# Optimization experiments

Hardware: AMD Instinct MI355X
Metric: run time of the kernel (lower is better)

Reference implementation:

```python
import jax, jax.numpy as jnp
import numpy as np

N_LAYERS = 2
D_MODEL = 1024
D_INNER = 2048  # expand=2
D_STATE = 16
D_CONV = 4
DT_RANK = 64    # ceil(d_model/16)
N_CLASSES = 10
B, L = 4, 1024


def setup_inputs() -> dict:
    key = jax.random.key(0)
    ks = jax.random.split(key, 20)
    s = 0.02
    inp = {
        'x': jax.random.normal(ks[0], (B, L, D_MODEL), jnp.float32),
        'ln1_w': jnp.ones((N_LAYERS, D_MODEL), jnp.float32),
        'ln1_b': jnp.zeros((N_LAYERS, D_MODEL), jnp.float32),
        'in_proj_w': jax.random.normal(ks[1], (N_LAYERS, 2 * D_INNER, D_MODEL), jnp.float32) * s,
        'conv_w': jax.random.normal(ks[2], (N_LAYERS, D_INNER, D_CONV), jnp.float32) * 0.2,
        'conv_b': jnp.zeros((N_LAYERS, D_INNER), jnp.float32),
        'x_proj_w': jax.random.normal(ks[3], (N_LAYERS, DT_RANK + 2 * D_STATE, D_INNER), jnp.float32) * s,
        'dt_proj_w': jax.random.normal(ks[4], (N_LAYERS, D_INNER, DT_RANK), jnp.float32) * 0.1,
        'dt_proj_b': jax.random.normal(ks[5], (N_LAYERS, D_INNER), jnp.float32) * 0.1 - 4.6,  # softplus -> dt ~ 0.01
        'A_log': jnp.broadcast_to(jnp.log(jnp.arange(1, D_STATE + 1, dtype=jnp.float32)), (N_LAYERS, D_INNER, D_STATE)) + 0.0,
        'D_param': jnp.ones((N_LAYERS, D_INNER), jnp.float32),
        'out_proj_w': jax.random.normal(ks[6], (N_LAYERS, D_MODEL, D_INNER), jnp.float32) * s,
        'norm_w': jnp.ones((D_MODEL,), jnp.float32),
        'norm_b': jnp.zeros((D_MODEL,), jnp.float32),
        'head_w': jax.random.normal(ks[7], (N_CLASSES, D_MODEL), jnp.float32) * s,
        'head_b': jnp.zeros((N_CLASSES,), jnp.float32),
    }
    return inp


def _layernorm(x, w, b, eps=1e-5):
    mu = jnp.mean(x, axis=-1, keepdims=True)
    var = jnp.var(x, axis=-1, keepdims=True)
    return (x - mu) * jax.lax.rsqrt(var + eps) * w + b


def _selective_scan(xc, dt, A, Bm, Cm, D):
    # xc, dt: (B, L, D_INNER); Bm, Cm: (B, L, D_STATE); A: (D_INNER, D_STATE); D: (D_INNER,)
    def step(h, inp):
        dt_t, B_t, C_t, xc_t = inp  # (B,C),(B,N),(B,N),(B,C)
        dA = jnp.exp(dt_t[..., None] * A)            # (B, C, N)
        h = dA * h + (dt_t * xc_t)[..., None] * B_t[:, None, :]
        y = jnp.einsum('bcn,bn->bc', h, C_t)
        return h, y

    h0 = jnp.zeros((xc.shape[0], A.shape[0], A.shape[1]), xc.dtype)
    xs = (dt.transpose(1, 0, 2), Bm.transpose(1, 0, 2), Cm.transpose(1, 0, 2), xc.transpose(1, 0, 2))
    _, ys = jax.lax.scan(step, h0, xs)
    y = ys.transpose(1, 0, 2)  # (B, L, C)
    return y + xc * D


def _mamba_layer(x, ln_w, ln_b, in_w, cw, cb, xp_w, dtp_w, dtp_b, A_log, D, out_w):
    h = _layernorm(x, ln_w, ln_b)
    xz = jnp.einsum('bld,ed->ble', h, in_w)          # (B, L, 2*D_INNER)
    x_in, z = jnp.split(xz, 2, axis=-1)
    # causal depthwise conv1d, kernel D_CONV
    xp = jnp.pad(x_in, ((0, 0), (D_CONV - 1, 0), (0, 0)))
    conv = cb
    for k in range(D_CONV):
        conv = conv + cw[:, k] * xp[:, k:k + x_in.shape[1], :]
    xc = jax.nn.silu(conv)
    x_dbl = jnp.einsum('blc,ec->ble', xc, xp_w)
    dt_r = x_dbl[..., :DT_RANK]
    Bm = x_dbl[..., DT_RANK:DT_RANK + D_STATE]
    Cm = x_dbl[..., DT_RANK + D_STATE:]
    dt = jax.nn.softplus(jnp.einsum('blr,cr->blc', dt_r, dtp_w) + dtp_b)
    A = -jnp.exp(A_log)
    y = _selective_scan(xc, dt, A, Bm, Cm, D)
    y = y * jax.nn.silu(z)
    return x + jnp.einsum('blc,dc->bld', y, out_w)


def reference(x, ln1_w, ln1_b, in_proj_w, conv_w, conv_b, x_proj_w, dt_proj_w, dt_proj_b,
              A_log, D_param, out_proj_w, norm_w, norm_b, head_w, head_b):
    for i in range(N_LAYERS):
        x = _mamba_layer(x, ln1_w[i], ln1_b[i], in_proj_w[i], conv_w[i], conv_b[i],
                         x_proj_w[i], dt_proj_w[i], dt_proj_b[i], A_log[i], D_param[i], out_proj_w[i])
    x = _layernorm(x, norm_w, norm_b)
    pooled = jnp.mean(x, axis=1)  # (B, D_MODEL)
    return pooled @ head_w.T + head_b
```

## Files before the change

kernel.cpp:

```cpp
#include <hip/hip_runtime.h>
#include <hip/hip_bf16.h>

#define N_LAYERS 2
#define D_MODEL 1024
#define D_INNER 2048
#define D_STATE 16
#define D_CONV 4
#define DT_RANK 64
#define N_CLASSES 10
#define BB 4
#define LL 1024
#define BL (BB*LL)
#define CH 32
#define CLEN (LL/CH)
#define KS 8
#define KSO 2

typedef __attribute__((ext_vector_type(8))) short bf16x8;
typedef __attribute__((ext_vector_type(8))) unsigned short us8;
typedef __attribute__((ext_vector_type(4))) float f32x4;

typedef const void __attribute__((address_space(1)))* gas_ptr;
typedef void __attribute__((address_space(3)))* las_ptr;
#define GLDS16(g, p) __builtin_amdgcn_global_load_lds((gas_ptr)(g), (las_ptr)(p), 16, 0, 0)

__device__ inline unsigned short rnd_bf16(float x) {
  unsigned u = __float_as_uint(x);
  return (unsigned short)((u + 0x7FFFu + ((u >> 16) & 1u)) >> 16);
}
__device__ inline float b2f(unsigned short u) {
  return __uint_as_float(((unsigned)u) << 16);
}

__global__ __launch_bounds__(256) void round_k(const float* __restrict__ in,
    unsigned short* __restrict__ hi) {
  const int i = blockIdx.x * 256 + threadIdx.x;
  const float4 v = ((const float4*)in)[i];
  ushort4 h4;
  h4.x = rnd_bf16(v.x); h4.y = rnd_bf16(v.y);
  h4.z = rnd_bf16(v.z); h4.w = rnd_bf16(v.w);
  ((ushort4*)hi)[i] = h4;
}

__global__ __launch_bounds__(256) void layernorm_bf16_k(const float* __restrict__ x,
    const float* __restrict__ w, const float* __restrict__ b,
    unsigned short* __restrict__ oh) {
  const int row = blockIdx.x;
  const int t = threadIdx.x;
  const float4 v = *(const float4*)(x + (size_t)row * D_MODEL + t * 4);
  float s = v.x + v.y + v.z + v.w;
  float q = v.x*v.x + v.y*v.y + v.z*v.z + v.w*v.w;
  #pragma unroll
  for (int o = 32; o; o >>= 1) { s += __shfl_down(s, o); q += __shfl_down(q, o); }
  __shared__ float red[8];
  if ((t & 63) == 0) { red[t >> 6] = s; red[4 + (t >> 6)] = q; }
  __syncthreads();
  s = red[0] + red[1] + red[2] + red[3];
  q = red[4] + red[5] + red[6] + red[7];
  const float mean = s * (1.f / D_MODEL);
  const float var  = q * (1.f / D_MODEL) - mean * mean;
  const float rstd = rsqrtf(var + 1e-5f);
  const float4 wv = *(const float4*)(w + t * 4);
  const float4 bv = *(const float4*)(b + t * 4);
  ushort4 h4;
  h4.x = rnd_bf16((v.x - mean) * rstd * wv.x + bv.x);
  h4.y = rnd_bf16((v.y - mean) * rstd * wv.y + bv.y);
  h4.z = rnd_bf16((v.z - mean) * rstd * wv.z + bv.z);
  h4.w = rnd_bf16((v.w - mean) * rstd * wv.w + bv.w);
  ((ushort4*)(oh + (size_t)row * D_MODEL))[t] = h4;
}

template<int OUT>
__global__ __launch_bounds__(256) void oreduce_ln_k(
    const float* __restrict__ part, const float* __restrict__ Xin,
    float* __restrict__ Xout,
    const float* __restrict__ w, const float* __restrict__ b,
    void* __restrict__ out) {
  const int row = blockIdx.x;
  const int t = threadIdx.x;
  float4 v = *(const float4*)(Xin + (size_t)row * D_MODEL + t * 4);
  #pragma unroll
  for (int k = 0; k < KSO; k++) {
    const float4 p = *(const float4*)(part + (size_t)k * BL * D_MODEL
                                      + (size_t)row * D_MODEL + t * 4);
    v.x += p.x; v.y += p.y; v.z += p.z; v.w += p.w;
  }
  *(float4*)(Xout + (size_t)row * D_MODEL + t * 4) = v;
  float s = v.x + v.y + v.z + v.w;
  float q = v.x*v.x + v.y*v.y + v.z*v.z + v.w*v.w;
  #pragma unroll
  for (int o = 32; o; o >>= 1) { s += __shfl_down(s, o); q += __shfl_down(q, o); }
  __shared__ float red[8];
  if ((t & 63) == 0) { red[t >> 6] = s; red[4 + (t >> 6)] = q; }
  __syncthreads();
  s = red[0] + red[1] + red[2] + red[3];
  q = red[4] + red[5] + red[6] + red[7];
  const float mean = s * (1.f / D_MODEL);
  const float var  = q * (1.f / D_MODEL) - mean * mean;
  const float rstd = rsqrtf(var + 1e-5f);
  const float4 wv = *(const float4*)(w + t * 4);
  const float4 bv = *(const float4*)(b + t * 4);
  float4 o4;
  o4.x = (v.x - mean) * rstd * wv.x + bv.x;
  o4.y = (v.y - mean) * rstd * wv.y + bv.y;
  o4.z = (v.z - mean) * rstd * wv.z + bv.z;
  o4.w = (v.w - mean) * rstd * wv.w + bv.w;
  if constexpr (OUT == 0) {
    ushort4 h4;
    h4.x = rnd_bf16(o4.x); h4.y = rnd_bf16(o4.y);
    h4.z = rnd_bf16(o4.z); h4.w = rnd_bf16(o4.w);
    ((ushort4*)((unsigned short*)out + (size_t)row * D_MODEL))[t] = h4;
  } else {
    *(float4*)((float*)out + (size_t)row * D_MODEL + t * 4) = o4;
  }
}

template<int EPI, int KSEG>
__global__ __launch_bounds__(256) void mfma_gemm_nt(
    const unsigned short* __restrict__ Ah, const unsigned short* __restrict__ Bh,
    void* __restrict__ Cv, int M, int N, int K, int ldc) {
  __shared__ unsigned short As[128 * 64];
  __shared__ unsigned short Bs[128 * 64];
  const int tid = threadIdx.x;
  const int w = tid >> 6, l = tid & 63;
  const int wr = w >> 1, wc = w & 1;
  const int m0 = blockIdx.y * 128, n0 = blockIdx.x * 128;
  const int kz = (KSEG > 1) ? blockIdx.z : 0;
  const int kbeg = kz * (K / KSEG);
  const int kend = kbeg + K / KSEG;
  const int srow = l >> 3;
  const int scol = (l & 7) * 8;
  const int fr = l & 15;
  const int fk = (l >> 4) * 8;
  f32x4 acc[4][4] = {};

  #pragma unroll 1
  for (int k0 = kbeg; k0 < kend; k0 += 64) {
    __syncthreads();
    #pragma unroll
    for (int it = 0; it < 4; ++it) {
      const int bi = it * 4 + w;
      const int row = bi * 8 + srow;
      GLDS16(Ah + (size_t)(m0 + row) * K + k0 + scol, &As[bi * 512 + l * 8]);
      GLDS16(Bh + (size_t)(n0 + row) * K + k0 + scol, &Bs[bi * 512 + l * 8]);
    }
    __syncthreads();
    #pragma unroll
    for (int kk = 0; kk < 64; kk += 32) {
      bf16x8 a[4], b[4];
      #pragma unroll
      for (int f = 0; f < 4; ++f)
        b[f] = *(const bf16x8*)&Bs[(wc * 64 + f * 16 + fr) * 64 + kk + fk];
      #pragma unroll
      for (int f = 0; f < 4; ++f)
        a[f] = *(const bf16x8*)&As[(wr * 64 + f * 16 + fr) * 64 + kk + fk];
      #pragma unroll
      for (int i = 0; i < 4; ++i)
        #pragma unroll
        for (int j = 0; j < 4; ++j)
          acc[i][j] = __builtin_amdgcn_mfma_f32_16x16x32_bf16(
              a[i], b[j], acc[i][j], 0, 0, 0);
    }
  }
  const int orow = (l >> 4) * 4;
  const int ocol = l & 15;
  if constexpr (EPI == 0) {
    unsigned short* Cw = (unsigned short*)Cv;
    #pragma unroll
    for (int i = 0; i < 4; ++i)
      #pragma unroll
      for (int j = 0; j < 4; ++j)
        #pragma unroll
        for (int r = 0; r < 4; ++r) {
          const int m = m0 + wr * 64 + i * 16 + orow + r;
          const int n = n0 + wc * 64 + j * 16 + ocol;
          Cw[(size_t)m * ldc + n] = rnd_bf16(acc[i][j][r]);
        }
  } else {
    float* Cw = (float*)Cv + (size_t)kz * M * ldc;
    #pragma unroll
    for (int i = 0; i < 4; ++i)
      #pragma unroll
      for (int j = 0; j < 4; ++j)
        #pragma unroll
        for (int r = 0; r < 4; ++r) {
          const int m = m0 + wr * 64 + i * 16 + orow + r;
          const int n = n0 + wc * 64 + j * 16 + ocol;
          Cw[(size_t)m * ldc + n] = acc[i][j][r];
        }
  }
}

template<int BM, int BN, int BK, int TM, int TN, int EPI>
__global__ __launch_bounds__(256) void sgemm_nt(
    const float* __restrict__ A, const float* __restrict__ B,
    float* __restrict__ C, int M, int N, int K, int lda, int ldb, int ldc,
    const float* __restrict__ bias) {
  constexpr int THREADS = 256;
  constexpr int NT = BN / TN;
  constexpr int K4 = BK / 4;
  constexpr int A_F4 = BM * BK / (THREADS * 4);
  constexpr int B_F4 = BN * BK / (THREADS * 4);
  static_assert((BM / TM) * (BN / TN) == THREADS, "thread shape");
  __shared__ float As[BK][BM + 4];
  __shared__ float Bs[BK][BN + 4];
  const int tid = threadIdx.x;
  const int m0 = blockIdx.y * BM;
  const int n0 = blockIdx.x * BN;
  const int tn = (tid % NT) * TN;
  const int tm = (tid / NT) * TM;
  float acc[TM][TN] = {};
  for (int k0 = 0; k0 < K; k0 += BK) {
    #pragma unroll
    for (int i = 0; i < A_F4; i++) {
      int li = tid + i * THREADS;
      int r = li / K4, c4 = li % K4;
      float4 v = *(const float4*)(A + (size_t)(m0 + r) * lda + k0 + c4 * 4);
      As[c4*4+0][r] = v.x; As[c4*4+1][r] = v.y; As[c4*4+2][r] = v.z; As[c4*4+3][r] = v.w;
    }
    #pragma unroll
    for (int i = 0; i < B_F4; i++) {
      int li = tid + i * THREADS;
      int r = li / K4, c4 = li % K4;
      float4 v = *(const float4*)(B + (size_t)(n0 + r) * ldb + k0 + c4 * 4);
      Bs[c4*4+0][r] = v.x; Bs[c4*4+1][r] = v.y; Bs[c4*4+2][r] = v.z; Bs[c4*4+3][r] = v.w;
    }
    __syncthreads();
    #pragma unroll
    for (int k = 0; k < BK; k++) {
      float a[TM], bf[TN];
      #pragma unroll
      for (int i = 0; i < TM; i++) a[i] = As[k][tm + i];
      #pragma unroll
      for (int j = 0; j < TN; j++) bf[j] = Bs[k][tn + j];
      #pragma unroll
      for (int i = 0; i < TM; i++)
        #pragma unroll
        for (int j = 0; j < TN; j++)
          acc[i][j] = fmaf(a[i], bf[j], acc[i][j]);
    }
    __syncthreads();
  }
  #pragma unroll
  for (int i = 0; i < TM; i++) {
    const int m = m0 + tm + i;
    #pragma unroll
    for (int j = 0; j < TN; j++) {
      const int n = n0 + tn + j;
      float v = acc[i][j];
      if constexpr (EPI == 1) {
        v += bias[n];
        v = (v > 20.f) ? v : log1pf(__expf(v));
      }
      C[(size_t)m * ldc + n] = v;
    }
  }
}

__global__ __launch_bounds__(256) void sgemm_splitk_k(
    const unsigned short* __restrict__ A, const float* __restrict__ B,
    float* __restrict__ part) {
  __shared__ float As[32][64 + 4];
  __shared__ float Bs[32][32 + 4];
  const int tid = threadIdx.x;
  const int n0 = blockIdx.x * 32;
  const int m0 = blockIdx.y * 64;
  const int kz = blockIdx.z;
  const int tn = (tid & 15) * 2;
  const int tm = (tid >> 4) * 4;
  float acc[4][2] = {};
  for (int kb = 0; kb < 256; kb += 32) {
    const int k0 = kz * 256 + kb;
    {
      int r = tid >> 2, c8 = (tid & 3) * 8;
      us8 u = *(const us8*)(A + (size_t)(m0 + r) * D_INNER + k0 + c8);
      #pragma unroll
      for (int j = 0; j < 8; j++) As[c8 + j][r] = b2f((unsigned short)u[j]);
    }
    {
      int r = tid >> 3, c4 = tid & 7;
      float4 v = *(const float4*)(B + (size_t)(n0 + r) * D_INNER + k0 + c4 * 4);
      Bs[c4*4+0][r] = v.x; Bs[c4*4+1][r] = v.y;
      Bs[c4*4+2][r] = v.z; Bs[c4*4+3][r] = v.w;
    }
    __syncthreads();
    #pragma unroll
    for (int k = 0; k < 32; k++) {
      float a[4], bf[2];
      #pragma unroll
      for (int i = 0; i < 4; i++) a[i] = As[k][tm + i];
      bf[0] = Bs[k][tn]; bf[1] = Bs[k][tn + 1];
      #pragma unroll
      for (int i = 0; i < 4; i++) {
        acc[i][0] = fmaf(a[i], bf[0], acc[i][0]);
        acc[i][1] = fmaf(a[i], bf[1], acc[i][1]);
      }
    }
    __syncthreads();
  }
  float* p = part + (size_t)kz * BL * 96;
  #pragma unroll
  for (int i = 0; i < 4; i++) {
    const int m = m0 + tm + i;
    p[(size_t)m * 96 + n0 + tn]     = acc[i][0];
    p[(size_t)m * 96 + n0 + tn + 1] = acc[i][1];
  }
}

__global__ __launch_bounds__(256) void xproj_reduce_k(
    const float* __restrict__ part, float* __restrict__ out) {
  const int i = blockIdx.x * 256 + threadIdx.x;
  float s = 0.f;
  #pragma unroll
  for (int k = 0; k < KS; k++) s += part[(size_t)k * BL * 96 + i];
  out[i] = s;
}

__global__ __launch_bounds__(256) void conv_silu_k(
    const unsigned short* __restrict__ xz,
    const float* __restrict__ cw, const float* __restrict__ cb,
    unsigned short* __restrict__ xc) {
  const int gid = blockIdx.x * 256 + threadIdx.x;
  const int c4 = (gid & (D_INNER / 4 - 1)) << 2;
  const int row = gid >> 9;
  const int l = row & (LL - 1);
  const unsigned short* base = xz + (size_t)row * (2 * D_INNER) + c4;
  const float4 w0 = *(const float4*)(cw + (c4 + 0) * 4);
  const float4 w1 = *(const float4*)(cw + (c4 + 1) * 4);
  const float4 w2 = *(const float4*)(cw + (c4 + 2) * 4);
  const float4 w3 = *(const float4*)(cw + (c4 + 3) * 4);
  float4 acc = *(const float4*)(cb + c4);
  ushort4 uv = *(const ushort4*)base;
  acc.x = fmaf(w0.w, b2f(uv.x), acc.x); acc.y = fmaf(w1.w, b2f(uv.y), acc.y);
  acc.z = fmaf(w2.w, b2f(uv.z), acc.z); acc.w = fmaf(w3.w, b2f(uv.w), acc.w);
  if (l >= 1) {
    uv = *(const ushort4*)(base - 2 * D_INNER);
    acc.x = fmaf(w0.z, b2f(uv.x), acc.x); acc.y = fmaf(w1.z, b2f(uv.y), acc.y);
    acc.z = fmaf(w2.z, b2f(uv.z), acc.z); acc.w = fmaf(w3.z, b2f(uv.w), acc.w);
  }
  if (l >= 2) {
    uv = *(const ushort4*)(base - 4 * D_INNER);
    acc.x = fmaf(w0.y, b2f(uv.x), acc.x); acc.y = fmaf(w1.y, b2f(uv.y), acc.y);
    acc.z = fmaf(w2.y, b2f(uv.z), acc.z); acc.w = fmaf(w3.y, b2f(uv.w), acc.w);
  }
  if (l >= 3) {
    uv = *(const ushort4*)(base - 6 * D_INNER);
    acc.x = fmaf(w0.x, b2f(uv.x), acc.x); acc.y = fmaf(w1.x, b2f(uv.y), acc.y);
    acc.z = fmaf(w2.x, b2f(uv.z), acc.z); acc.w = fmaf(w3.x, b2f(uv.w), acc.w);
  }
  ushort4 o4;
  o4.x = rnd_bf16(acc.x / (1.f + __expf(-acc.x)));
  o4.y = rnd_bf16(acc.y / (1.f + __expf(-acc.y)));
  o4.z = rnd_bf16(acc.z / (1.f + __expf(-acc.z)));
  o4.w = rnd_bf16(acc.w / (1.f + __expf(-acc.w)));
  *(ushort4*)(xc + (size_t)row * D_INNER + c4) = o4;
}

__global__ __launch_bounds__(256) void scan_pass1_k(
    const float* __restrict__ dt, const unsigned short* __restrict__ xc,
    const float* __restrict__ xdbl, const float* __restrict__ A_log,
    float* __restrict__ hend, float* __restrict__ sumdt) {
  const int c = blockIdx.x * 256 + threadIdx.x;
  const int k = blockIdx.y;
  const int b = blockIdx.z;
  float Ac[D_STATE];
  #pragma unroll
  for (int n = 0; n < D_STATE; n++) Ac[n] = -__expf(A_log[c * D_STATE + n]);
  float h[D_STATE] = {};
  float sd = 0.f;
  const size_t r0 = (size_t)b * LL + (size_t)k * CLEN;
  const float* dtp = dt + r0 * D_INNER + c;
  const unsigned short* xcp = xc + r0 * D_INNER + c;
  const float* Bp  = xdbl + r0 * 96 + DT_RANK;

  float dtv = dtp[0];
  float xv  = b2f(xcp[0]);
  float4 B0 = *(const float4*)(Bp + 0);
  float4 B1 = *(const float4*)(Bp + 4);
  float4 B2 = *(const float4*)(Bp + 8);
  float4 B3 = *(const float4*)(Bp + 12);
  for (int l = 0; l < CLEN; l++) {
    const int lp = (l + 1 < CLEN) ? l + 1 : l;
    const float dtv2 = dtp[(size_t)lp * D_INNER];
    const float xv2  = b2f(xcp[(size_t)lp * D_INNER]);
    const float4 B0n = *(const float4*)(Bp + (size_t)lp * 96 + 0);
    const float4 B1n = *(const float4*)(Bp + (size_t)lp * 96 + 4);
    const float4 B2n = *(const float4*)(Bp + (size_t)lp * 96 + 8);
    const float4 B3n = *(const float4*)(Bp + (size_t)lp * 96 + 12);
    sd += dtv;
    const float dx = dtv * xv;
    const float Bv[D_STATE] = {B0.x,B0.y,B0.z,B0.w, B1.x,B1.y,B1.z,B1.w,
                               B2.x,B2.y,B2.z,B2.w, B3.x,B3.y,B3.z,B3.w};
    #pragma unroll
    for (int n = 0; n < D_STATE; n++)
      h[n] = fmaf(__expf(dtv * Ac[n]), h[n], dx * Bv[n]);
    dtv = dtv2; xv = xv2; B0 = B0n; B1 = B1n; B2 = B2n; B3 = B3n;
  }
  float* he = hend + (((size_t)(b * CH + k) * D_INNER + c) << 4);
  #pragma unroll
  for (int n = 0; n < D_STATE; n += 4)
    *(float4*)(he + n) = make_float4(h[n], h[n+1], h[n+2], h[n+3]);
  sumdt[(size_t)(b * CH + k) * D_INNER + c] = sd;
}

__global__ __launch_bounds__(256) void scan_fix_k(
    float* __restrict__ hend, const float* __restrict__ sumdt,
    const float* __restrict__ A_log) {
  const int gid = blockIdx.x * 256 + threadIdx.x;
  const int n = gid & 15;
  const int c = (gid >> 4) & (D_INNER - 1);
  const int b = gid >> 15;
  const float Ac = -__expf(A_log[c * D_STATE + n]);
  float hrun = 0.f;
  for (int k = 0; k < CH; k++) {
    const size_t base = (size_t)(b * CH + k) * D_INNER + c;
    const float sd = sumdt[base];
    float* hp = hend + (base << 4) + n;
    const float tmp = *hp;
    *hp = hrun;
    hrun = fmaf(__expf(Ac * sd), hrun, tmp);
  }
}

__global__ __launch_bounds__(256) void scan_pass3_k(
    const float* __restrict__ dt, const unsigned short* __restrict__ xc,
    const float* __restrict__ xdbl, const unsigned short* __restrict__ xz,
    const float* __restrict__ h0, const float* __restrict__ A_log,
    const float* __restrict__ Dp, unsigned short* __restrict__ yh) {
  const int c = blockIdx.x * 256 + threadIdx.x;
  const int k = blockIdx.y;
  const int b = blockIdx.z;
  float Ac[D_STATE];
  #pragma unroll
  for (int n = 0; n < D_STATE; n++) Ac[n] = -__expf(A_log[c * D_STATE + n]);
  const float Dv = Dp[c];
  float h[D_STATE];
  const float* hp = h0 + (((size_t)(b * CH + k) * D_INNER + c) << 4);
  #pragma unroll
  for (int n = 0; n < D_STATE; n += 4) {
    const float4 v = *(const float4*)(hp + n);
    h[n] = v.x; h[n+1] = v.y; h[n+2] = v.z; h[n+3] = v.w;
  }
  const size_t r0 = (size_t)b * LL + (size_t)k * CLEN;
  const float* dtp = dt + r0 * D_INNER + c;
  const unsigned short* xcp = xc + r0 * D_INNER + c;
  const float* Bp  = xdbl + r0 * 96 + DT_RANK;
  const unsigned short* zp = xz + r0 * (size_t)(2 * D_INNER) + D_INNER + c;
  unsigned short* yhp = yh + r0 * D_INNER + c;

  float dtv = dtp[0];
  float xv  = b2f(xcp[0]);
  float zv  = b2f(zp[0]);
  float4 B0 = *(const float4*)(Bp + 0);
  float4 B1 = *(const float4*)(Bp + 4);
  float4 B2 = *(const float4*)(Bp + 8);
  float4 B3 = *(const float4*)(Bp + 12);
  float4 C0 = *(const float4*)(Bp + 16);
  float4 C1 = *(const float4*)(Bp + 20);
  float4 C2 = *(const float4*)(Bp + 24);
  float4 C3 = *(const float4*)(Bp + 28);
  for (int l = 0; l < CLEN; l++) {
    const int lp = (l + 1 < CLEN) ? l + 1 : l;
    const float dtv2 = dtp[(size_t)lp * D_INNER];
    const float xv2  = b2f(xcp[(size_t)lp * D_INNER]);
    const float zv2  = b2f(zp[(size_t)lp * 2 * D_INNER]);
    const float4 B0n = *(const float4*)(Bp + (size_t)lp * 96 + 0);
    const float4 B1n = *(const float4*)(Bp + (size_t)lp * 96 + 4);
    const float4 B2n = *(const float4*)(Bp + (size_t)lp * 96 + 8);
    const float4 B3n = *(const float4*)(Bp + (size_t)lp * 96 + 12);
    const float4 C0n = *(const float4*)(Bp + (size_t)lp * 96 + 16);
    const float4 C1n = *(const float4*)(Bp + (size_t)lp * 96 + 20);
    const float4 C2n = *(const float4*)(Bp + (size_t)lp * 96 + 24);
    const float4 C3n = *(const float4*)(Bp + (size_t)lp * 96 + 28);
    const float dx = dtv * xv;
    const float Bv[D_STATE] = {B0.x,B0.y,B0.z,B0.w, B1.x,B1.y,B1.z,B1.w,
                               B2.x,B2.y,B2.z,B2.w, B3.x,B3.y,B3.z,B3.w};
    const float Cv[D_STATE] = {C0.x,C0.y,C0.z,C0.w, C1.x,C1.y,C1.z,C1.w,
                               C2.x,C2.y,C2.z,C2.w, C3.x,C3.y,C3.z,C3.w};
    float y = 0.f;
    #pragma unroll
    for (int n = 0; n < D_STATE; n++) {
      h[n] = fmaf(__expf(dtv * Ac[n]), h[n], dx * Bv[n]);
      y = fmaf(h[n], Cv[n], y);
    }
    y = fmaf(xv, Dv, y);
    y *= zv / (1.f + __expf(-zv));
    yhp[(size_t)l * D_INNER] = rnd_bf16(y);
    dtv = dtv2; xv = xv2; zv = zv2;
    B0 = B0n; B1 = B1n; B2 = B2n; B3 = B3n;
    C0 = C0n; C1 = C1n; C2 = C2n; C3 = C3n;
  }
}

__global__ __launch_bounds__(256) void pool1_k(const float* __restrict__ h,
    float* __restrict__ pp) {
  const int d = blockIdx.x * 256 + threadIdx.x;
  const int b = blockIdx.y;
  const int seg = blockIdx.z;
  float s = 0.f;
  const size_t base = (size_t)b * LL + (size_t)seg * 64;
  for (int l = 0; l < 64; l++) s += h[(base + l) * D_MODEL + d];
  pp[((size_t)(b * 16 + seg)) * D_MODEL + d] = s;
}
__global__ __launch_bounds__(256) void pool2_k(const float* __restrict__ pp,
    float* __restrict__ pooled) {
  const int d = blockIdx.x * 256 + threadIdx.x;
  const int b = blockIdx.y;
  float s = 0.f;
  #pragma unroll
  for (int k = 0; k < 16; k++) s += pp[((size_t)(b * 16 + k)) * D_MODEL + d];
  pooled[b * D_MODEL + d] = s * (1.f / LL);
}

__global__ __launch_bounds__(64) void head_k(const float* __restrict__ pooled,
    const float* __restrict__ hw, const float* __restrict__ hb,
    float* __restrict__ out) {
  const int b = blockIdx.x / N_CLASSES;
  const int j = blockIdx.x % N_CLASSES;
  float s = 0.f;
  for (int k = threadIdx.x; k < D_MODEL; k += 64)
    s = fmaf(pooled[b * D_MODEL + k], hw[j * D_MODEL + k], s);
  #pragma unroll
  for (int o = 32; o; o >>= 1) s += __shfl_down(s, o);
  if (threadIdx.x == 0) out[b * N_CLASSES + j] = s + hb[j];
}

extern "C" void kernel_launch(void* const* d_in, const int* in_sizes, int n_in,
                              void* d_out, int out_size, void* d_ws, size_t ws_size,
                              hipStream_t stream) {
  const float* x0    = (const float*)d_in[0];
  const float* ln1w  = (const float*)d_in[1];
  const float* ln1b  = (const float*)d_in[2];
  const float* inw   = (const float*)d_in[3];
  const float* convw = (const float*)d_in[4];
  const float* convb = (const float*)d_in[5];
  const float* xpw   = (const float*)d_in[6];
  const float* dtpw  = (const float*)d_in[7];
  const float* dtpb  = (const float*)d_in[8];
  const float* Alog  = (const float*)d_in[9];
  const float* Dp    = (const float*)d_in[10];
  const float* outw  = (const float*)d_in[11];
  const float* normw = (const float*)d_in[12];
  const float* normb = (const float*)d_in[13];
  const float* headw = (const float*)d_in[14];
  const float* headb = (const float*)d_in[15];

  float* ws = (float*)d_ws;
  size_t f = 0;
  float* X      = ws + f; f += (size_t)BL * D_MODEL;
  float* xzf    = ws + f; f += (size_t)BL * D_INNER;
  float* xdbl   = ws + f; f += (size_t)BL * 96;
  float* dty    = ws + f; f += (size_t)BL * D_INNER;
  float* pooled = ws + f; f += 4096;
  float* pooldp = ws + f; f += (size_t)16 * BB * D_MODEL;
  float* xpart  = ws + f; f += (size_t)KS * BL * 96;
  float* hend   = ws + f; f += (size_t)BB * CH * D_INNER * D_STATE;
  float* opart  = ws + f; f += (size_t)KSO * BL * D_MODEL;
  unsigned short* hh  = (unsigned short*)(ws + f); f += (size_t)BL * D_MODEL / 2;
  unsigned short* yh  = (unsigned short*)(ws + f); f += (size_t)BL * D_INNER / 2;
  unsigned short* xcb = (unsigned short*)(ws + f); f += (size_t)BL * D_INNER / 2;
  unsigned short* wih = (unsigned short*)(ws + f);
  f += (size_t)N_LAYERS * 2 * D_INNER * D_MODEL / 2;
  unsigned short* woh = (unsigned short*)(ws + f);
  f += (size_t)N_LAYERS * D_MODEL * D_INNER / 2;
  unsigned short* xz = (unsigned short*)xzf;
  float* sumdt = xpart;

  round_k<<<(N_LAYERS * 2 * D_INNER * D_MODEL) / 1024, 256, 0, stream>>>(inw, wih);
  round_k<<<(N_LAYERS * D_MODEL * D_INNER) / 1024, 256, 0, stream>>>(outw, woh);
  layernorm_bf16_k<<<BL, 256, 0, stream>>>(x0, ln1w, ln1b, hh);

  for (int layer = 0; layer < N_LAYERS; ++layer) {
    const unsigned short* wi = wih + (size_t)layer * 2 * D_INNER * D_MODEL;
    const unsigned short* wo = woh + (size_t)layer * D_MODEL * D_INNER;
    mfma_gemm_nt<0, 1><<<dim3(4096 / 128, 4096 / 128), 256, 0, stream>>>(
        hh, wi, xz, BL, 2 * D_INNER, D_MODEL, 2 * D_INNER);
    conv_silu_k<<<(BL * D_INNER / 4) / 256, 256, 0, stream>>>(
        xz, convw + layer * D_INNER * D_CONV, convb + layer * D_INNER, xcb);
    sgemm_splitk_k<<<dim3(96 / 32, 4096 / 64, KS), 256, 0, stream>>>(
        xcb, xpw + (size_t)layer * 96 * D_INNER, xpart);
    xproj_reduce_k<<<(BL * 96) / 256, 256, 0, stream>>>(xpart, xdbl);
    sgemm_nt<64,64,64,4,4,1><<<dim3(2048 / 64, 4096 / 64), 256, 0, stream>>>(
        xdbl, dtpw + (size_t)layer * D_INNER * DT_RANK, dty,
        BL, D_INNER, DT_RANK, 96, DT_RANK, D_INNER,
        dtpb + layer * D_INNER);
    scan_pass1_k<<<dim3(D_INNER / 256, CH, BB), 256, 0, stream>>>(
        dty, xcb, xdbl, Alog + (size_t)layer * D_INNER * D_STATE, hend, sumdt);
    scan_fix_k<<<(BB * D_INNER * D_STATE) / 256, 256, 0, stream>>>(
        hend, sumdt, Alog + (size_t)layer * D_INNER * D_STATE);
    scan_pass3_k<<<dim3(D_INNER / 256, CH, BB), 256, 0, stream>>>(
        dty, xcb, xdbl, xz, hend, Alog + (size_t)layer * D_INNER * D_STATE,
        Dp + layer * D_INNER, yh);
    mfma_gemm_nt<1, KSO><<<dim3(1024 / 128, 4096 / 128, KSO), 256, 0, stream>>>(
        yh, wo, opart, BL, D_MODEL, D_INNER, D_MODEL);
    const float* Xin = (layer == 0) ? x0 : X;
    if (layer + 1 < N_LAYERS) {
      oreduce_ln_k<0><<<BL, 256, 0, stream>>>(
          opart, Xin, X, ln1w + (layer + 1) * D_MODEL,
          ln1b + (layer + 1) * D_MODEL, hh);
    } else {
      oreduce_ln_k<1><<<BL, 256, 0, stream>>>(opart, Xin, X, normw, normb, dty);
    }
  }

  pool1_k<<<dim3(D_MODEL / 256, BB, 16), 256, 0, stream>>>(dty, pooldp);
  pool2_k<<<dim3(D_MODEL / 256, BB), 256, 0, stream>>>(pooldp, pooled);
  head_k<<<BB * N_CLASSES, 64, 0, stream>>>(pooled, headw, headb, (float*)d_out);
}
```

Measured before the change: 609.4 us.

## Store dt in bf16 and swizzle MFMA GEMM block order across XCDs

The dt projection epilogue now writes softplus output as bf16, and both scan passes read bf16 dt, which halves dt traffic in the memory-bound scan kernels. The MFMA GEMM also remaps block IDs so that consecutive workgroups on each XCD cover an 8x8 tile group, aiming for better L2 reuse of A/B panels. The cost is lower precision for dt, and the remap assumes the grid dimensions divide by 8 and by 64 workgroups.

```diff
diff --git a/kernel.cpp b/kernel.cpp
--- a/kernel.cpp
+++ b/kernel.cpp
@@ -124,7 +124,14 @@
   const int tid = threadIdx.x;
   const int w = tid >> 6, l = tid & 63;
   const int wr = w >> 1, wc = w & 1;
-  const int m0 = blockIdx.y * 128, n0 = blockIdx.x * 128;
+  const int nbx = gridDim.x;
+  const int nwg = nbx * gridDim.y;
+  int bid = blockIdx.y * nbx + blockIdx.x;
+  bid = (bid & 7) * (nwg >> 3) + (bid >> 3);
+  const int st = bid >> 6, wi = bid & 63;
+  const int stpr = nbx >> 3;
+  const int n0 = ((st % stpr) * 8 + (wi & 7)) * 128;
+  const int m0 = ((st / stpr) * 8 + (wi >> 3)) * 128;
   const int kz = (KSEG > 1) ? blockIdx.z : 0;
   const int kbeg = kz * (K / KSEG);
   const int kend = kbeg + K / KSEG;
@@ -194,7 +201,7 @@
 template<int BM, int BN, int BK, int TM, int TN, int EPI>
 __global__ __launch_bounds__(256) void sgemm_nt(
     const float* __restrict__ A, const float* __restrict__ B,
-    float* __restrict__ C, int M, int N, int K, int lda, int ldb, int ldc,
+    void* __restrict__ Cv, int M, int N, int K, int lda, int ldb, int ldc,
     const float* __restrict__ bias) {
   constexpr int THREADS = 256;
   constexpr int NT = BN / TN;
@@ -251,8 +258,10 @@
       if constexpr (EPI == 1) {
         v += bias[n];
         v = (v > 20.f) ? v : log1pf(__expf(v));
+        ((unsigned short*)Cv)[(size_t)m * ldc + n] = rnd_bf16(v);
+      } else {
+        ((float*)Cv)[(size_t)m * ldc + n] = v;
       }
-      C[(size_t)m * ldc + n] = v;
     }
   }
 }
@@ -357,7 +366,7 @@
 }
 
 __global__ __launch_bounds__(256) void scan_pass1_k(
-    const float* __restrict__ dt, const unsigned short* __restrict__ xc,
+    const unsigned short* __restrict__ dt, const unsigned short* __restrict__ xc,
     const float* __restrict__ xdbl, const float* __restrict__ A_log,
     float* __restrict__ hend, float* __restrict__ sumdt) {
   const int c = blockIdx.x * 256 + threadIdx.x;
@@ -369,11 +378,11 @@
   float h[D_STATE] = {};
   float sd = 0.f;
   const size_t r0 = (size_t)b * LL + (size_t)k * CLEN;
-  const float* dtp = dt + r0 * D_INNER + c;
+  const unsigned short* dtp = dt + r0 * D_INNER + c;
   const unsigned short* xcp = xc + r0 * D_INNER + c;
   const float* Bp  = xdbl + r0 * 96 + DT_RANK;
 
-  float dtv = dtp[0];
+  float dtv = b2f(dtp[0]);
   float xv  = b2f(xcp[0]);
   float4 B0 = *(const float4*)(Bp + 0);
   float4 B1 = *(const float4*)(Bp + 4);
@@ -381,7 +390,7 @@
   float4 B3 = *(const float4*)(Bp + 12);
   for (int l = 0; l < CLEN; l++) {
     const int lp = (l + 1 < CLEN) ? l + 1 : l;
-    const float dtv2 = dtp[(size_t)lp * D_INNER];
+    const float dtv2 = b2f(dtp[(size_t)lp * D_INNER]);
     const float xv2  = b2f(xcp[(size_t)lp * D_INNER]);
     const float4 B0n = *(const float4*)(Bp + (size_t)lp * 96 + 0);
     const float4 B1n = *(const float4*)(Bp + (size_t)lp * 96 + 4);
@@ -423,7 +432,7 @@
 }
 
 __global__ __launch_bounds__(256) void scan_pass3_k(
-    const float* __restrict__ dt, const unsigned short* __restrict__ xc,
+    const unsigned short* __restrict__ dt, const unsigned short* __restrict__ xc,
     const float* __restrict__ xdbl, const unsigned short* __restrict__ xz,
     const float* __restrict__ h0, const float* __restrict__ A_log,
     const float* __restrict__ Dp, unsigned short* __restrict__ yh) {
@@ -442,13 +451,13 @@
     h[n] = v.x; h[n+1] = v.y; h[n+2] = v.z; h[n+3] = v.w;
   }
   const size_t r0 = (size_t)b * LL + (size_t)k * CLEN;
-  const float* dtp = dt + r0 * D_INNER + c;
+  const unsigned short* dtp = dt + r0 * D_INNER + c;
   const unsigned short* xcp = xc + r0 * D_INNER + c;
   const float* Bp  = xdbl + r0 * 96 + DT_RANK;
   const unsigned short* zp = xz + r0 * (size_t)(2 * D_INNER) + D_INNER + c;
   unsigned short* yhp = yh + r0 * D_INNER + c;
 
-  float dtv = dtp[0];
+  float dtv = b2f(dtp[0]);
   float xv  = b2f(xcp[0]);
   float zv  = b2f(zp[0]);
   float4 B0 = *(const float4*)(Bp + 0);
@@ -461,7 +470,7 @@
   float4 C3 = *(const float4*)(Bp + 28);
   for (int l = 0; l < CLEN; l++) {
     const int lp = (l + 1 < CLEN) ? l + 1 : l;
-    const float dtv2 = dtp[(size_t)lp * D_INNER];
+    const float dtv2 = b2f(dtp[(size_t)lp * D_INNER]);
     const float xv2  = b2f(xcp[(size_t)lp * D_INNER]);
     const float zv2  = b2f(zp[(size_t)lp * 2 * D_INNER]);
     const float4 B0n = *(const float4*)(Bp + (size_t)lp * 96 + 0);
@@ -563,7 +572,8 @@
   f += (size_t)N_LAYERS * 2 * D_INNER * D_MODEL / 2;
   unsigned short* woh = (unsigned short*)(ws + f);
   f += (size_t)N_LAYERS * D_MODEL * D_INNER / 2;
-  unsigned short* xz = (unsigned short*)xzf;
+  unsigned short* xz  = (unsigned short*)xzf;
+  unsigned short* dtb = (unsigned short*)dty;
   float* sumdt = xpart;
 
   round_k<<<(N_LAYERS * 2 * D_INNER * D_MODEL) / 1024, 256, 0, stream>>>(inw, wih);
@@ -581,15 +591,15 @@
         xcb, xpw + (size_t)layer * 96 * D_INNER, xpart);
     xproj_reduce_k<<<(BL * 96) / 256, 256, 0, stream>>>(xpart, xdbl);
     sgemm_nt<64,64,64,4,4,1><<<dim3(2048 / 64, 4096 / 64), 256, 0, stream>>>(
-        xdbl, dtpw + (size_t)layer * D_INNER * DT_RANK, dty,
+        xdbl, dtpw + (size_t)layer * D_INNER * DT_RANK, dtb,
         BL, D_INNER, DT_RANK, 96, DT_RANK, D_INNER,
         dtpb + layer * D_INNER);
     scan_pass1_k<<<dim3(D_INNER / 256, CH, BB), 256, 0, stream>>>(
-        dty, xcb, xdbl, Alog + (size_t)layer * D_INNER * D_STATE, hend, sumdt);
+        dtb, xcb, xdbl, Alog + (size_t)layer * D_INNER * D_STATE, hend, sumdt);
     scan_fix_k<<<(BB * D_INNER * D_STATE) / 256, 256, 0, stream>>>(
         hend, sumdt, Alog + (size_t)layer * D_INNER * D_STATE);
     scan_pass3_k<<<dim3(D_INNER / 256, CH, BB), 256, 0, stream>>>(
-        dty, xcb, xdbl, xz, hend, Alog + (size_t)layer * D_INNER * D_STATE,
+        dtb, xcb, xdbl, xz, hend, Alog + (size_t)layer * D_INNER * D_STATE,
         Dp + layer * D_INNER, yh);
     mfma_gemm_nt<1, KSO><<<dim3(1024 / 128, 4096 / 128, KSO), 256, 0, stream>>>(
         yh, wo, opart, BL, D_MODEL, D_INNER, D_MODEL);
```

Result: no change. 603.2 us (-1.0%).
